# Kernel tuning notes

Hardware: AMD Instinct MI355X
Metric: run time of the kernel (lower is better)

Reference implementation:

```python
import jax, jax.numpy as jnp
import numpy as np

V, NB, NJ, NP, NK = 6890, 10, 24, 207, 19
PARENTS = np.array([-1, 0, 0, 0, 1, 2, 3, 4, 5, 6, 7, 8, 9, 9, 9, 12, 13, 14, 16, 17, 18, 19, 20, 21])


def setup_inputs():
    key = jax.random.key(0)
    ks = jax.random.split(key, 9)
    B = 1024
    beta = jax.random.normal(ks[0], (B, NB), jnp.float32)
    theta = jax.random.normal(ks[1], (B, NJ * 3), jnp.float32) * 0.3  # axis-angle per joint
    trans = jax.random.normal(ks[2], (B, 3), jnp.float32)
    v_template = jax.random.normal(ks[3], (V, 3), jnp.float32)
    shapedirs = jax.random.normal(ks[4], (NB, V * 3), jnp.float32) * 0.03
    Jr = jax.random.uniform(ks[5], (V, NJ), jnp.float32)
    J_regressor = Jr / jnp.sum(Jr, axis=0, keepdims=True)
    posedirs = jax.random.normal(ks[6], (NP, V * 3), jnp.float32) * 0.01
    jr = jax.random.uniform(ks[7], (V, NK), jnp.float32)
    joint_regressor = jr / jnp.sum(jr, axis=0, keepdims=True)
    w = jax.random.uniform(ks[8], (V, NJ), jnp.float32)
    weights = w / jnp.sum(w, axis=1, keepdims=True)  # LBS weights, rows sum to 1
    return dict(beta=beta, theta=theta, trans=trans, v_template=v_template,
                shapedirs=shapedirs, J_regressor=J_regressor, posedirs=posedirs,
                joint_regressor=joint_regressor, weights=weights)


def batch_rodrigues(theta):
    # theta: (N,3) axis-angle -> (N,3,3) rotation matrices via quaternions (HMR-style)
    angle = jnp.linalg.norm(theta + 1e-8, axis=1, keepdims=True)
    half = angle * 0.5
    v = (theta / angle) * jnp.sin(half)
    quat = jnp.concatenate([jnp.cos(half), v], axis=1)
    quat = quat / jnp.linalg.norm(quat, axis=1, keepdims=True)
    w, x, y, z = quat[:, 0], quat[:, 1], quat[:, 2], quat[:, 3]
    rot = jnp.stack([
        1 - 2 * (y * y + z * z), 2 * (x * y - w * z), 2 * (x * z + w * y),
        2 * (x * y + w * z), 1 - 2 * (x * x + z * z), 2 * (y * z - w * x),
        2 * (x * z - w * y), 2 * (y * z + w * x), 1 - 2 * (x * x + y * y)], axis=1)
    return rot.reshape(-1, 3, 3)


def batch_global_rigid_transformation(Rs, J):
    # Rs: (B,24,3,3), J: (B,24,3); rotate_base=True
    B = Rs.shape[0]
    rot_x = jnp.array([[1., 0., 0.], [0., -1., 0.], [0., 0., -1.]], jnp.float32)
    root_R = Rs[:, 0] @ rot_x

    def make_A(R, t):  # (B,3,3),(B,3) -> (B,4,4)
        top = jnp.concatenate([R, t[:, :, None]], axis=2)
        bot = jnp.broadcast_to(jnp.array([0., 0., 0., 1.], jnp.float32), (B, 1, 4))
        return jnp.concatenate([top, bot], axis=1)

    results = [make_A(root_R, J[:, 0])]
    for i in range(1, NJ):  # fixed 24-joint kinematic chain
        t = J[:, i] - J[:, PARENTS[i]]
        results.append(results[PARENTS[i]] @ make_A(Rs[:, i], t))
    res = jnp.stack(results, axis=1)  # (B,24,4,4)
    new_J = res[:, :, :3, 3]
    j_w0 = jnp.concatenate([J, jnp.zeros_like(J[:, :, :1])], axis=2)  # (B,24,4), homo w=0
    init_bone = jnp.einsum('bjrc,bjc->bjr', res, j_w0)
    A = res.at[:, :, :, 3].add(-init_bone)  # subtract only last column (matches F.pad trick)
    return new_J, A


def reference(beta, theta, trans, v_template, shapedirs, J_regressor, posedirs, joint_regressor, weights):
    B = beta.shape[0]
    v_shaped = (beta @ shapedirs).reshape(B, V, 3) + v_template
    J = jnp.einsum('bvc,vj->bjc', v_shaped, J_regressor)  # (B,24,3)
    Rs = batch_rodrigues(theta.reshape(-1, 3)).reshape(B, NJ, 3, 3)
    pose_feature = (Rs[:, 1:] - jnp.eye(3, dtype=Rs.dtype)).reshape(B, NP)
    v_posed = (pose_feature @ posedirs).reshape(B, V, 3) + v_shaped
    _, A = batch_global_rigid_transformation(Rs, J)
    T = jnp.einsum('vj,bjrc->bvrc', weights, A)  # (B,V,4,4) per-vertex skinning transforms
    homo = jnp.concatenate([v_posed, jnp.ones((B, V, 1), v_posed.dtype)], axis=2)
    verts = jnp.einsum('bvrc,bvc->bvr', T, homo)[:, :, :3] + trans[:, None, :]
    joints = jnp.einsum('bvc,vk->bkc', verts, joint_regressor)  # (B,19,3)
    return joints
```

## Files before the change

kernel.cpp:

```cpp
#include <hip/hip_runtime.h>
#include <hip/hip_bf16.h>

constexpr int Vn   = 6890;
constexpr int VC3  = 20670;
constexpr int KP   = 6912;
constexpr int NKB  = 216;
constexpr int QT   = 224;
constexpr int NMG  = 14;
constexpr int NCOL = 480;
constexpr int WR   = 1440;
constexpr int MC   = 1368;
constexpr int KSEG = 8;
constexpr int NG3  = 88;

using bf16x8  = __attribute__((ext_vector_type(8))) short;
using floatx4 = __attribute__((ext_vector_type(4))) float;

__device__ __forceinline__ unsigned short f2bf(float f) {
    unsigned int u = __float_as_uint(f);
    unsigned int r = (u + 0x7FFFu + ((u >> 16) & 1u)) >> 16;
    return (unsigned short)r;
}

__global__ __launch_bounds__(256) void k0_build(
    const float* __restrict__ vt, const float* __restrict__ sdirs,
    const float* __restrict__ pdirs, const float* __restrict__ Jreg,
    const float* __restrict__ jreg, const float* __restrict__ wts,
    unsigned short* __restrict__ Af, unsigned short* __restrict__ Bf)
{
    int bx = blockIdx.x, t = threadIdx.x;
    if (bx < QT * 27) {
        int q = bx / 27, v = (bx % 27) * 256 + t;
        float f[3] = {0.f, 0.f, 0.f};
        if (v < Vn) {
            if (q == 0) { f[0] = f[1] = f[2] = 1.f; }
            else {
                const float* src = nullptr;
                if (q == 1) src = vt;
                else if (q >= 2 && q < 12)   src = sdirs + (size_t)(q - 2) * VC3;
                else if (q >= 12 && q < 219) src = pdirs + (size_t)(q - 12) * VC3;
                if (src) { f[0] = src[3 * v]; f[1] = src[3 * v + 1]; f[2] = src[3 * v + 2]; }
            }
        }
        int mg = q >> 4, kb = v >> 5;
        size_t off = (size_t)((q & 15) + ((v >> 3) & 3) * 16) * 8 + (v & 7);
        #pragma unroll
        for (int c = 0; c < 3; ++c)
            Af[((size_t)(c * NMG + mg) * NKB + kb) * 512 + off] = f2bf(f[c]);
        return;
    }
    bx -= QT * 27;
    int v0 = bx * 64;
    __shared__ float js[64 * 19], wsh[64 * 24], Jsh[64 * 24];
    for (int i = t; i < 64 * 19; i += 256)
        js[i] = (v0 * 19 + i < Vn * 19) ? jreg[v0 * 19 + i] : 0.f;
    for (int i = t; i < 64 * 24; i += 256) {
        wsh[i] = (v0 * 24 + i < Vn * 24) ? wts[v0 * 24 + i] : 0.f;
        Jsh[i] = (v0 * 24 + i < Vn * 24) ? Jreg[v0 * 24 + i] : 0.f;
    }
    __syncthreads();
    for (int s = t; s < 4096; s += 256) {
        int col = s >> 3, vg = s & 7;
        int kb = (v0 >> 5) + (vg >> 2);
        bf16x8 o;
        #pragma unroll
        for (int j = 0; j < 8; ++j) {
            int vl = vg * 8 + j;
            float val = 0.f;
            if (col < 456)      val = js[vl * 19 + col / 24] * wsh[vl * 24 + col % 24];
            else if (col < 480) val = Jsh[vl * 24 + (col - 456)];
            o[j] = (short)f2bf(val);
        }
        *(bf16x8*)(Bf + ((size_t)(col >> 4) * NKB + kb) * 512
                      + (size_t)((col & 15) + (vg & 3) * 16) * 8) = o;
    }
}

__device__ __forceinline__ void k1_load(bf16x8 (&a)[2], bf16x8 (&b)[4],
    const unsigned short* __restrict__ ap, const unsigned short* __restrict__ bp, int i)
{
    a[0] = *(const bf16x8*)(ap + (size_t)(0 * NKB + i) * 512);
    a[1] = *(const bf16x8*)(ap + (size_t)(1 * NKB + i) * 512);
    b[0] = *(const bf16x8*)(bp + (size_t)(0 * NKB + i) * 512);
    b[1] = *(const bf16x8*)(bp + (size_t)(1 * NKB + i) * 512);
    b[2] = *(const bf16x8*)(bp + (size_t)(2 * NKB + i) * 512);
    b[3] = *(const bf16x8*)(bp + (size_t)(3 * NKB + i) * 512);
}

__global__ __launch_bounds__(64) void k1_mfma(
    const unsigned short* __restrict__ Af, const unsigned short* __restrict__ Bf,
    float* __restrict__ P)
{
    int l = threadIdx.x;
    int wid = blockIdx.x;
    int kseg = wid / 168; int r = wid % 168;
    int c = r / 56; r %= 56;
    int mt = r >> 3, nt = r & 7;
    int kb0 = kseg * 27;

    const unsigned short* ap = Af + ((size_t)(c * NMG + mt * 2) * NKB + kb0) * 512 + l * 8;
    const unsigned short* bp = Bf + ((size_t)(nt * 4) * NKB + kb0) * 512 + l * 8;

    floatx4 acc[2][4];
    #pragma unroll
    for (int mi = 0; mi < 2; ++mi)
        #pragma unroll
        for (int ni = 0; ni < 4; ++ni) acc[mi][ni] = floatx4{0.f, 0.f, 0.f, 0.f};

    bf16x8 a[4][2], b[4][4];
    k1_load(a[0], b[0], ap, bp, 0);
    k1_load(a[1], b[1], ap, bp, 1);
    k1_load(a[2], b[2], ap, bp, 2);
    #pragma unroll
    for (int i = 0; i < 27; ++i) {
        int pf = (i + 3 < 27) ? i + 3 : 26;
        k1_load(a[(i + 3) & 3], b[(i + 3) & 3], ap, bp, pf);
        bf16x8 (&ac)[2] = a[i & 3];
        bf16x8 (&bc)[4] = b[i & 3];
        #pragma unroll
        for (int mi = 0; mi < 2; ++mi)
            #pragma unroll
            for (int ni = 0; ni < 4; ++ni)
                acc[mi][ni] = __builtin_amdgcn_mfma_f32_16x16x32_bf16(ac[mi], bc[ni], acc[mi][ni], 0, 0, 0);
    }
    float* Ps = P + (size_t)kseg * WR * QT;
    int lr = l & 15, r0 = (l >> 4) * 4;
    #pragma unroll
    for (int mi = 0; mi < 2; ++mi)
        #pragma unroll
        for (int ni = 0; ni < 4; ++ni) {
            int col = nt * 64 + ni * 16 + lr;
            if (col < NCOL) {
                int q0 = mt * 32 + mi * 16 + r0;
                #pragma unroll
                for (int rr = 0; rr < 4; ++rr)
                    Ps[(size_t)(col * 3 + c) * QT + q0 + rr] = acc[mi][ni][rr];
            }
        }
}

constexpr int RB = 158;
__global__ __launch_bounds__(256) void k12_reduce_prep(
    const float* __restrict__ P,
    const float* __restrict__ beta, const float* __restrict__ theta,
    float* __restrict__ WtF, unsigned short* __restrict__ Wb3,
    unsigned short* __restrict__ xbf, float* __restrict__ RAg, float* __restrict__ tAg)
{
    int t = threadIdx.x;
    if (blockIdx.x < RB) {
        int g = blockIdx.x * 256 + t;
        if (g >= WR * 28) return;
        int colc = g / 28, qg = g % 28, q0 = qg * 8;
        float v[8] = {0, 0, 0, 0, 0, 0, 0, 0};
        #pragma unroll
        for (int s = 0; s < KSEG; ++s) {
            const float4* p = (const float4*)(P + ((size_t)s * WR + colc) * QT + q0);
            float4 x0 = p[0], x1 = p[1];
            v[0] += x0.x; v[1] += x0.y; v[2] += x0.z; v[3] += x0.w;
            v[4] += x1.x; v[5] += x1.y; v[6] += x1.z; v[7] += x1.w;
        }
        float4* wp = (float4*)(WtF + (size_t)colc * QT + q0);
        wp[0] = make_float4(v[0], v[1], v[2], v[3]);
        wp[1] = make_float4(v[4], v[5], v[6], v[7]);
        if (colc < NG3 * 16) {
            bf16x8 o;
            #pragma unroll
            for (int j = 0; j < 8; ++j)
                o[j] = (short)((colc < MC) ? f2bf(v[j]) : 0);
            int ng3 = colc >> 4, kb3 = q0 >> 5;
            *(bf16x8*)(Wb3 + ((size_t)ng3 * 7 + kb3) * 512
                           + (size_t)((colc & 15) + ((q0 >> 3) & 3) * 16) * 8) = o;
        }
        return;
    }
    int b = blockIdx.x - RB;
    __shared__ float Rs[24][9];
    __shared__ float Jl[24][3];
    __shared__ float resR[24][9];
    __shared__ float rest[24][3];
    __shared__ float bet[10];

    if (t < 10) bet[t] = beta[b * 10 + t];
    if (t < 24) {
        float t0 = theta[b * 72 + t * 3 + 0];
        float t1 = theta[b * 72 + t * 3 + 1];
        float t2 = theta[b * 72 + t * 3 + 2];
        float e0 = t0 + 1e-8f, e1 = t1 + 1e-8f, e2 = t2 + 1e-8f;
        float angle = sqrtf(e0 * e0 + e1 * e1 + e2 * e2);
        float half = 0.5f * angle;
        float sh = sinf(half), ch = cosf(half);
        float s = sh / angle;
        float qx = t0 * s, qy = t1 * s, qz = t2 * s;
        float qn = sqrtf(ch * ch + qx * qx + qy * qy + qz * qz);
        float w = ch / qn, x = qx / qn, y = qy / qn, z = qz / qn;
        Rs[t][0] = 1.f - 2.f * (y * y + z * z);
        Rs[t][1] = 2.f * (x * y - w * z);
        Rs[t][2] = 2.f * (x * z + w * y);
        Rs[t][3] = 2.f * (x * y + w * z);
        Rs[t][4] = 1.f - 2.f * (x * x + z * z);
        Rs[t][5] = 2.f * (y * z - w * x);
        Rs[t][6] = 2.f * (x * z + -w * y);
        Rs[t][7] = 2.f * (y * z + w * x);
        Rs[t][8] = 1.f - 2.f * (x * x + y * y);
    }
    __syncthreads();
    if (t < 72) {
        int colc = 1368 + t;
        float acc = 0.f;
        #pragma unroll
        for (int s = 0; s < KSEG; ++s)
            acc += P[((size_t)s * WR + colc) * QT + 1];
        #pragma unroll
        for (int n = 0; n < 10; ++n) {
            float cf = 0.f;
            #pragma unroll
            for (int s = 0; s < KSEG; ++s)
                cf += P[((size_t)s * WR + colc) * QT + 2 + n];
            acc += bet[n] * cf;
        }
        Jl[t / 3][t % 3] = acc;
    }
    if (t < QT) {
        int q = t;
        float xv = 0.f;
        if (q == 1) xv = 1.f;
        else if (q >= 2 && q < 12) xv = bet[q - 2];
        else if (q >= 12 && q < 219) {
            int p = q - 12;
            int jj = 1 + p / 9, e = p % 9;
            float rr = Rs[jj][e];
            if (e == 0 || e == 4 || e == 8) rr -= 1.f;
            xv = rr;
        }
        int bg = b >> 4, kb3 = q >> 5;
        xbf[((size_t)bg * 7 + kb3) * 512
            + (size_t)((b & 15) + ((q >> 3) & 3) * 16) * 8 + (q & 7)] = f2bf(xv);
    }
    __syncthreads();
    if (t == 0) {
        const int par[24] = {-1,0,0,0,1,2,3,4,5,6,7,8,9,9,9,12,13,14,16,17,18,19,20,21};
        #pragma unroll
        for (int rr = 0; rr < 3; ++rr) {
            resR[0][rr * 3 + 0] =  Rs[0][rr * 3 + 0];
            resR[0][rr * 3 + 1] = -Rs[0][rr * 3 + 1];
            resR[0][rr * 3 + 2] = -Rs[0][rr * 3 + 2];
            rest[0][rr] = Jl[0][rr];
        }
        for (int i = 1; i < 24; ++i) {
            int p = par[i];
            float t0 = Jl[i][0] - Jl[p][0];
            float t1 = Jl[i][1] - Jl[p][1];
            float t2 = Jl[i][2] - Jl[p][2];
            #pragma unroll
            for (int rr = 0; rr < 3; ++rr) {
                float a0 = resR[p][rr * 3 + 0], a1 = resR[p][rr * 3 + 1], a2 = resR[p][rr * 3 + 2];
                resR[i][rr * 3 + 0] = a0 * Rs[i][0] + a1 * Rs[i][3] + a2 * Rs[i][6];
                resR[i][rr * 3 + 1] = a0 * Rs[i][1] + a1 * Rs[i][4] + a2 * Rs[i][7];
                resR[i][rr * 3 + 2] = a0 * Rs[i][2] + a1 * Rs[i][5] + a2 * Rs[i][8];
                rest[i][rr] = a0 * t0 + a1 * t1 + a2 * t2 + rest[p][rr];
            }
        }
    }
    __syncthreads();
    if (t < 216) RAg[(size_t)b * 216 + t] = resR[t / 9][t % 9];
    if (t < 72) {
        int j = t / 3, c = t % 3;
        tAg[(size_t)b * 72 + t] = rest[j][c]
            - (resR[j][c * 3 + 0] * Jl[j][0] + resR[j][c * 3 + 1] * Jl[j][1]
             + resR[j][c * 3 + 2] * Jl[j][2]);
    }
}

__device__ __forceinline__ void k3_load(bf16x8 (&a)[2], bf16x8 (&b)[4],
    const unsigned short* __restrict__ ap, const unsigned short* __restrict__ bp, int i)
{
    a[0] = *(const bf16x8*)(ap + (size_t)(0 * 7 + i) * 512);
    a[1] = *(const bf16x8*)(ap + (size_t)(1 * 7 + i) * 512);
    b[0] = *(const bf16x8*)(bp + (size_t)(0 * 7 + i) * 512);
    b[1] = *(const bf16x8*)(bp + (size_t)(1 * 7 + i) * 512);
    b[2] = *(const bf16x8*)(bp + (size_t)(2 * 7 + i) * 512);
    b[3] = *(const bf16x8*)(bp + (size_t)(3 * 7 + i) * 512);
}

__global__ __launch_bounds__(256) void k3_mfma(
    const unsigned short* __restrict__ xbf, const unsigned short* __restrict__ Wb3,
    float* __restrict__ Mg)
{
    int w = threadIdx.x >> 6, l = threadIdx.x & 63;
    int wm = w & 1, wn = w >> 1;
    int bt = blockIdx.x / 11, ct = blockIdx.x % 11;
    int bg0 = bt * 4 + wm * 2;
    int ng0 = ct * 8 + wn * 4;

    const unsigned short* ap = xbf + (size_t)bg0 * 7 * 512 + l * 8;
    const unsigned short* bp = Wb3 + (size_t)ng0 * 7 * 512 + l * 8;

    floatx4 acc[2][4];
    #pragma unroll
    for (int mi = 0; mi < 2; ++mi)
        #pragma unroll
        for (int ni = 0; ni < 4; ++ni) acc[mi][ni] = floatx4{0.f, 0.f, 0.f, 0.f};

    bf16x8 a[3][2], b[3][4];
    k3_load(a[0], b[0], ap, bp, 0);
    k3_load(a[1], b[1], ap, bp, 1);
    #pragma unroll
    for (int i = 0; i < 7; ++i) {
        int pf = (i + 2 < 7) ? i + 2 : 6;
        k3_load(a[(i + 2) % 3], b[(i + 2) % 3], ap, bp, pf);
        bf16x8 (&ac)[2] = a[i % 3];
        bf16x8 (&bc)[4] = b[i % 3];
        #pragma unroll
        for (int mi = 0; mi < 2; ++mi)
            #pragma unroll
            for (int ni = 0; ni < 4; ++ni)
                acc[mi][ni] = __builtin_amdgcn_mfma_f32_16x16x32_bf16(ac[mi], bc[ni], acc[mi][ni], 0, 0, 0);
    }
    int lr = l & 15, r0 = (l >> 4) * 4;
    #pragma unroll
    for (int mi = 0; mi < 2; ++mi)
        #pragma unroll
        for (int ni = 0; ni < 4; ++ni) {
            int cc = ct * 128 + wn * 64 + ni * 16 + lr;
            if (cc < MC) {
                int brow = bt * 64 + wm * 32 + mi * 16 + r0;
                #pragma unroll
                for (int rr = 0; rr < 4; ++rr)
                    Mg[(size_t)(brow + rr) * MC + cc] = acc[mi][ni][rr];
            }
        }
}

__global__ __launch_bounds__(256) void k4_combine(
    const float* __restrict__ Mg, const float* __restrict__ RAg,
    const float* __restrict__ tAg, const float* __restrict__ WtF,
    const float* __restrict__ trans, float* __restrict__ out)
{
    __shared__ float w1s[456];
    __shared__ float Ms[4 * MC];
    __shared__ float RAs[4 * 216];
    __shared__ float tAs[4 * 72];
    int tid = threadIdx.x;
    int b0 = blockIdx.x * 4;
    for (int i = tid; i < 456; i += 256) w1s[i] = WtF[(size_t)i * 3 * QT];
    for (int i = tid; i < 4 * MC; i += 256) Ms[i] = Mg[(size_t)b0 * MC + i];
    for (int i = tid; i < 4 * 216; i += 256) RAs[i] = RAg[(size_t)b0 * 216 + i];
    for (int i = tid; i < 4 * 72; i += 256) tAs[i] = tAg[(size_t)b0 * 72 + i];
    __syncthreads();
    if (tid < 228) {
        int lb = tid / 57, kc = tid % 57;
        int k = kc / 3, c = kc % 3;
        int b = b0 + lb;
        float acc = trans[b * 3 + c];
        const float* Mrow = Ms + lb * MC;
        const float* RAr  = RAs + lb * 216;
        const float* tAr  = tAs + lb * 72;
        #pragma unroll
        for (int j = 0; j < 24; ++j) {
            int kj = k * 24 + j;
            float m0 = Mrow[kj * 3 + 0], m1 = Mrow[kj * 3 + 1], m2 = Mrow[kj * 3 + 2];
            acc += RAr[j * 9 + c * 3 + 0] * m0
                 + RAr[j * 9 + c * 3 + 1] * m1
                 + RAr[j * 9 + c * 3 + 2] * m2
                 + tAr[j * 3 + c] * w1s[kj];
        }
        out[b * 57 + kc] = acc;
    }
}

extern "C" void kernel_launch(void* const* d_in, const int* in_sizes, int n_in,
                              void* d_out, int out_size, void* d_ws, size_t ws_size,
                              hipStream_t stream)
{
    const float* beta  = (const float*)d_in[0];
    const float* theta = (const float*)d_in[1];
    const float* trans = (const float*)d_in[2];
    const float* vt    = (const float*)d_in[3];
    const float* sdirs = (const float*)d_in[4];
    const float* Jreg  = (const float*)d_in[5];
    const float* pdirs = (const float*)d_in[6];
    const float* jreg  = (const float*)d_in[7];
    const float* wts   = (const float*)d_in[8];
    float* out = (float*)d_out;
    int B = in_sizes[0] / 10;

    unsigned short* Af  = (unsigned short*)d_ws;
    unsigned short* Bf  = Af + (size_t)3 * NMG * NKB * 512;
    unsigned short* Wb3 = Bf + (size_t)32 * NKB * 512;
    unsigned short* xbf = Wb3 + (size_t)NG3 * 7 * 512;
    float* P   = (float*)(xbf + (size_t)64 * 7 * 512);
    float* WtF = P + (size_t)KSEG * WR * QT;
    float* RAg = WtF + (size_t)WR * QT;
    float* tAg = RAg + (size_t)B * 216;
    float* Mg  = tAg + (size_t)B * 72;

    k0_build<<<dim3(QT * 27 + 108), 256, 0, stream>>>(
        vt, sdirs, pdirs, Jreg, jreg, wts, Af, Bf);
    k1_mfma<<<dim3(168 * KSEG), 64, 0, stream>>>(Af, Bf, P);
    k12_reduce_prep<<<dim3(RB + B), 256, 0, stream>>>(
        P, beta, theta, WtF, Wb3, xbf, RAg, tAg);
    k3_mfma<<<dim3((B / 64) * 11), 256, 0, stream>>>(xbf, Wb3, Mg);
    k4_combine<<<dim3(B / 4), 256, 0, stream>>>(Mg, RAg, tAg, WtF, trans, out);
}
```

Before: 153.6 us.

## Vectorize weight packing, share B tiles across xyz, split reduce/prep, transpose k3

The packing kernel now has each thread load 8 vertices with float2 reads and write whole bf16x8 fragments, where before it issued scalar strided stores. k1 computes all three coordinate channels in one wave so each B fragment is reused three times, with 12 K segments and double buffering, and writes results as vector stores. The fused reduce/prep kernel is split into a reduce kernel and a 64-thread per-batch prep kernel that reads the already reduced WtF instead of summing partials. k3 swaps operand roles so its outputs can be stored as float4. This adds a kernel launch and more partial-sum traffic from the extra segments.

```diff
diff --git a/kernel.cpp b/kernel.cpp
--- a/kernel.cpp
+++ b/kernel.cpp
@@ -3,14 +3,14 @@
 
 constexpr int Vn   = 6890;
 constexpr int VC3  = 20670;
-constexpr int KP   = 6912;
 constexpr int NKB  = 216;
 constexpr int QT   = 224;
 constexpr int NMG  = 14;
 constexpr int NCOL = 480;
 constexpr int WR   = 1440;
 constexpr int MC   = 1368;
-constexpr int KSEG = 8;
+constexpr int KSEG = 12;
+constexpr int KCH  = 18;
 constexpr int NG3  = 88;
 
 using bf16x8  = __attribute__((ext_vector_type(8))) short;
@@ -29,27 +29,43 @@
     unsigned short* __restrict__ Af, unsigned short* __restrict__ Bf)
 {
     int bx = blockIdx.x, t = threadIdx.x;
-    if (bx < QT * 27) {
-        int q = bx / 27, v = (bx % 27) * 256 + t;
-        float f[3] = {0.f, 0.f, 0.f};
-        if (v < Vn) {
-            if (q == 0) { f[0] = f[1] = f[2] = 1.f; }
-            else {
-                const float* src = nullptr;
-                if (q == 1) src = vt;
-                else if (q >= 2 && q < 12)   src = sdirs + (size_t)(q - 2) * VC3;
-                else if (q >= 12 && q < 219) src = pdirs + (size_t)(q - 12) * VC3;
-                if (src) { f[0] = src[3 * v]; f[1] = src[3 * v + 1]; f[2] = src[3 * v + 2]; }
+    if (bx < 756) {
+        int g = bx * 256 + t;
+        int q = g / 864, u = g % 864;
+        int v0 = u * 8, base = 3 * v0;
+        float buf[24];
+        if (q == 0) {
+            #pragma unroll
+            for (int i = 0; i < 24; ++i) buf[i] = (v0 + i / 3 < Vn) ? 1.f : 0.f;
+        } else {
+            const float* src = nullptr;
+            if (q == 1) src = vt;
+            else if (q >= 2 && q < 12)   src = sdirs + (size_t)(q - 2) * VC3;
+            else if (q >= 12 && q < 219) src = pdirs + (size_t)(q - 12) * VC3;
+            if (src && base + 23 < VC3) {
+                #pragma unroll
+                for (int i = 0; i < 12; ++i) {
+                    float2 f = *(const float2*)(src + base + 2 * i);
+                    buf[2 * i] = f.x; buf[2 * i + 1] = f.y;
+                }
+            } else {
+                #pragma unroll
+                for (int i = 0; i < 24; ++i)
+                    buf[i] = (src && base + i < VC3) ? src[base + i] : 0.f;
             }
         }
-        int mg = q >> 4, kb = v >> 5;
-        size_t off = (size_t)((q & 15) + ((v >> 3) & 3) * 16) * 8 + (v & 7);
-        #pragma unroll
-        for (int c = 0; c < 3; ++c)
-            Af[((size_t)(c * NMG + mg) * NKB + kb) * 512 + off] = f2bf(f[c]);
+        int kb = u >> 2, quad = u & 3, mg = q >> 4;
+        size_t foff = (size_t)((q & 15) + quad * 16) * 8;
+        #pragma unroll
+        for (int c = 0; c < 3; ++c) {
+            bf16x8 o;
+            #pragma unroll
+            for (int j = 0; j < 8; ++j) o[j] = (short)f2bf(buf[3 * j + c]);
+            *(bf16x8*)(Af + ((size_t)(c * NMG + mg) * NKB + kb) * 512 + foff) = o;
+        }
         return;
     }
-    bx -= QT * 27;
+    bx -= 756;
     int v0 = bx * 64;
     __shared__ float js[64 * 19], wsh[64 * 24], Jsh[64 * 24];
     for (int i = t; i < 64 * 19; i += 256)
@@ -76,115 +92,117 @@
     }
 }
 
-__device__ __forceinline__ void k1_load(bf16x8 (&a)[2], bf16x8 (&b)[4],
-    const unsigned short* __restrict__ ap, const unsigned short* __restrict__ bp, int i)
-{
-    a[0] = *(const bf16x8*)(ap + (size_t)(0 * NKB + i) * 512);
-    a[1] = *(const bf16x8*)(ap + (size_t)(1 * NKB + i) * 512);
-    b[0] = *(const bf16x8*)(bp + (size_t)(0 * NKB + i) * 512);
-    b[1] = *(const bf16x8*)(bp + (size_t)(1 * NKB + i) * 512);
-    b[2] = *(const bf16x8*)(bp + (size_t)(2 * NKB + i) * 512);
-    b[3] = *(const bf16x8*)(bp + (size_t)(3 * NKB + i) * 512);
-}
-
 __global__ __launch_bounds__(64) void k1_mfma(
     const unsigned short* __restrict__ Af, const unsigned short* __restrict__ Bf,
     float* __restrict__ P)
 {
     int l = threadIdx.x;
     int wid = blockIdx.x;
-    int kseg = wid / 168; int r = wid % 168;
-    int c = r / 56; r %= 56;
+    int kseg = wid / 56, r = wid % 56;
     int mt = r >> 3, nt = r & 7;
-    int kb0 = kseg * 27;
-
-    const unsigned short* ap = Af + ((size_t)(c * NMG + mt * 2) * NKB + kb0) * 512 + l * 8;
+    int kb0 = kseg * KCH;
+
+    const unsigned short* ap = Af + ((size_t)(mt * 2) * NKB + kb0) * 512 + l * 8;
     const unsigned short* bp = Bf + ((size_t)(nt * 4) * NKB + kb0) * 512 + l * 8;
 
-    floatx4 acc[2][4];
-    #pragma unroll
-    for (int mi = 0; mi < 2; ++mi)
-        #pragma unroll
-        for (int ni = 0; ni < 4; ++ni) acc[mi][ni] = floatx4{0.f, 0.f, 0.f, 0.f};
-
-    bf16x8 a[4][2], b[4][4];
-    k1_load(a[0], b[0], ap, bp, 0);
-    k1_load(a[1], b[1], ap, bp, 1);
-    k1_load(a[2], b[2], ap, bp, 2);
-    #pragma unroll
-    for (int i = 0; i < 27; ++i) {
-        int pf = (i + 3 < 27) ? i + 3 : 26;
-        k1_load(a[(i + 3) & 3], b[(i + 3) & 3], ap, bp, pf);
-        bf16x8 (&ac)[2] = a[i & 3];
-        bf16x8 (&bc)[4] = b[i & 3];
+    floatx4 acc[3][2][4];
+    #pragma unroll
+    for (int c = 0; c < 3; ++c)
         #pragma unroll
         for (int mi = 0; mi < 2; ++mi)
             #pragma unroll
+            for (int ni = 0; ni < 4; ++ni) acc[c][mi][ni] = floatx4{0.f, 0.f, 0.f, 0.f};
+
+    bf16x8 a[2][3][2], b[2][4];
+    #pragma unroll
+    for (int c = 0; c < 3; ++c)
+        #pragma unroll
+        for (int mi = 0; mi < 2; ++mi)
+            a[0][c][mi] = *(const bf16x8*)(ap + ((size_t)(c * NMG + mi) * NKB) * 512);
+    #pragma unroll
+    for (int ni = 0; ni < 4; ++ni)
+        b[0][ni] = *(const bf16x8*)(bp + ((size_t)ni * NKB) * 512);
+
+    for (int i = 0; i < KCH; ++i) {
+        int s = i & 1;
+        if (i + 1 < KCH) {
+            #pragma unroll
+            for (int c = 0; c < 3; ++c)
+                #pragma unroll
+                for (int mi = 0; mi < 2; ++mi)
+                    a[s ^ 1][c][mi] = *(const bf16x8*)(ap + ((size_t)(c * NMG + mi) * NKB + i + 1) * 512);
+            #pragma unroll
             for (int ni = 0; ni < 4; ++ni)
-                acc[mi][ni] = __builtin_amdgcn_mfma_f32_16x16x32_bf16(ac[mi], bc[ni], acc[mi][ni], 0, 0, 0);
-    }
-    float* Ps = P + (size_t)kseg * WR * QT;
-    int lr = l & 15, r0 = (l >> 4) * 4;
-    #pragma unroll
-    for (int mi = 0; mi < 2; ++mi)
-        #pragma unroll
-        for (int ni = 0; ni < 4; ++ni) {
-            int col = nt * 64 + ni * 16 + lr;
-            if (col < NCOL) {
-                int q0 = mt * 32 + mi * 16 + r0;
+                b[s ^ 1][ni] = *(const bf16x8*)(bp + ((size_t)ni * NKB + i + 1) * 512);
+        }
+        #pragma unroll
+        for (int c = 0; c < 3; ++c)
+            #pragma unroll
+            for (int mi = 0; mi < 2; ++mi)
                 #pragma unroll
-                for (int rr = 0; rr < 4; ++rr)
-                    Ps[(size_t)(col * 3 + c) * QT + q0 + rr] = acc[mi][ni][rr];
+                for (int ni = 0; ni < 4; ++ni)
+                    acc[c][mi][ni] = __builtin_amdgcn_mfma_f32_16x16x32_bf16(
+                        a[s][c][mi], b[s][ni], acc[c][mi][ni], 0, 0, 0);
+    }
+    float* base = P + (size_t)kseg * WR * QT;
+    int lr = l & 15, rq = (l >> 4) * 4;
+    #pragma unroll
+    for (int c = 0; c < 3; ++c)
+        #pragma unroll
+        for (int mi = 0; mi < 2; ++mi)
+            #pragma unroll
+            for (int ni = 0; ni < 4; ++ni) {
+                int col = nt * 64 + ni * 16 + lr;
+                if (col < NCOL) {
+                    int q0 = mt * 32 + mi * 16 + rq;
+                    *(floatx4*)(base + (size_t)(col * 3 + c) * QT + q0) = acc[c][mi][ni];
+                }
             }
-        }
-}
-
-constexpr int RB = 158;
-__global__ __launch_bounds__(256) void k12_reduce_prep(
-    const float* __restrict__ P,
+}
+
+__global__ __launch_bounds__(256) void kr_reduce(
+    const float* __restrict__ P, float* __restrict__ WtF, unsigned short* __restrict__ Wb3)
+{
+    int g = blockIdx.x * 256 + threadIdx.x;
+    if (g >= WR * 28) return;
+    int colc = g / 28, q0 = (g % 28) * 8;
+    float v[8] = {0, 0, 0, 0, 0, 0, 0, 0};
+    for (int s = 0; s < KSEG; ++s) {
+        const float4* p = (const float4*)(P + ((size_t)s * WR + colc) * QT + q0);
+        float4 x0 = p[0], x1 = p[1];
+        v[0] += x0.x; v[1] += x0.y; v[2] += x0.z; v[3] += x0.w;
+        v[4] += x1.x; v[5] += x1.y; v[6] += x1.z; v[7] += x1.w;
+    }
+    float4* wp = (float4*)(WtF + (size_t)colc * QT + q0);
+    wp[0] = make_float4(v[0], v[1], v[2], v[3]);
+    wp[1] = make_float4(v[4], v[5], v[6], v[7]);
+    if (colc < NG3 * 16) {
+        bf16x8 o;
+        #pragma unroll
+        for (int j = 0; j < 8; ++j)
+            o[j] = (short)((colc < MC) ? f2bf(v[j]) : 0);
+        *(bf16x8*)(Wb3 + ((size_t)(colc >> 4) * 7 + (q0 >> 5)) * 512
+                       + (size_t)((colc & 15) + ((q0 >> 3) & 3) * 16) * 8) = o;
+    }
+}
+
+__global__ __launch_bounds__(64) void kp_prep(
     const float* __restrict__ beta, const float* __restrict__ theta,
-    float* __restrict__ WtF, unsigned short* __restrict__ Wb3,
+    const float* __restrict__ WtF,
     unsigned short* __restrict__ xbf, float* __restrict__ RAg, float* __restrict__ tAg)
 {
-    int t = threadIdx.x;
-    if (blockIdx.x < RB) {
-        int g = blockIdx.x * 256 + t;
-        if (g >= WR * 28) return;
-        int colc = g / 28, qg = g % 28, q0 = qg * 8;
-        float v[8] = {0, 0, 0, 0, 0, 0, 0, 0};
-        #pragma unroll
-        for (int s = 0; s < KSEG; ++s) {
-            const float4* p = (const float4*)(P + ((size_t)s * WR + colc) * QT + q0);
-            float4 x0 = p[0], x1 = p[1];
-            v[0] += x0.x; v[1] += x0.y; v[2] += x0.z; v[3] += x0.w;
-            v[4] += x1.x; v[5] += x1.y; v[6] += x1.z; v[7] += x1.w;
-        }
-        float4* wp = (float4*)(WtF + (size_t)colc * QT + q0);
-        wp[0] = make_float4(v[0], v[1], v[2], v[3]);
-        wp[1] = make_float4(v[4], v[5], v[6], v[7]);
-        if (colc < NG3 * 16) {
-            bf16x8 o;
-            #pragma unroll
-            for (int j = 0; j < 8; ++j)
-                o[j] = (short)((colc < MC) ? f2bf(v[j]) : 0);
-            int ng3 = colc >> 4, kb3 = q0 >> 5;
-            *(bf16x8*)(Wb3 + ((size_t)ng3 * 7 + kb3) * 512
-                           + (size_t)((colc & 15) + ((q0 >> 3) & 3) * 16) * 8) = o;
-        }
-        return;
-    }
-    int b = blockIdx.x - RB;
+    int b = blockIdx.x, lane = threadIdx.x;
     __shared__ float Rs[24][9];
     __shared__ float Jl[24][3];
     __shared__ float resR[24][9];
     __shared__ float rest[24][3];
     __shared__ float bet[10];
 
-    if (t < 10) bet[t] = beta[b * 10 + t];
-    if (t < 24) {
-        float t0 = theta[b * 72 + t * 3 + 0];
-        float t1 = theta[b * 72 + t * 3 + 1];
-        float t2 = theta[b * 72 + t * 3 + 2];
+    if (lane < 10) bet[lane] = beta[b * 10 + lane];
+    if (lane < 24) {
+        float t0 = theta[b * 72 + lane * 3 + 0];
+        float t1 = theta[b * 72 + lane * 3 + 1];
+        float t2 = theta[b * 72 + lane * 3 + 2];
         float e0 = t0 + 1e-8f, e1 = t1 + 1e-8f, e2 = t2 + 1e-8f;
         float angle = sqrtf(e0 * e0 + e1 * e1 + e2 * e2);
         float half = 0.5f * angle;
@@ -193,35 +211,25 @@
         float qx = t0 * s, qy = t1 * s, qz = t2 * s;
         float qn = sqrtf(ch * ch + qx * qx + qy * qy + qz * qz);
         float w = ch / qn, x = qx / qn, y = qy / qn, z = qz / qn;
-        Rs[t][0] = 1.f - 2.f * (y * y + z * z);
-        Rs[t][1] = 2.f * (x * y - w * z);
-        Rs[t][2] = 2.f * (x * z + w * y);
-        Rs[t][3] = 2.f * (x * y + w * z);
-        Rs[t][4] = 1.f - 2.f * (x * x + z * z);
-        Rs[t][5] = 2.f * (y * z - w * x);
-        Rs[t][6] = 2.f * (x * z + -w * y);
-        Rs[t][7] = 2.f * (y * z + w * x);
-        Rs[t][8] = 1.f - 2.f * (x * x + y * y);
-    }
-    __syncthreads();
-    if (t < 72) {
-        int colc = 1368 + t;
-        float acc = 0.f;
-        #pragma unroll
-        for (int s = 0; s < KSEG; ++s)
-            acc += P[((size_t)s * WR + colc) * QT + 1];
-        #pragma unroll
-        for (int n = 0; n < 10; ++n) {
-            float cf = 0.f;
-            #pragma unroll
-            for (int s = 0; s < KSEG; ++s)
-                cf += P[((size_t)s * WR + colc) * QT + 2 + n];
-            acc += bet[n] * cf;
-        }
-        Jl[t / 3][t % 3] = acc;
-    }
-    if (t < QT) {
-        int q = t;
+        Rs[lane][0] = 1.f - 2.f * (y * y + z * z);
+        Rs[lane][1] = 2.f * (x * y - w * z);
+        Rs[lane][2] = 2.f * (x * z + w * y);
+        Rs[lane][3] = 2.f * (x * y + w * z);
+        Rs[lane][4] = 1.f - 2.f * (x * x + z * z);
+        Rs[lane][5] = 2.f * (y * z - w * x);
+        Rs[lane][6] = 2.f * (x * z - w * y);
+        Rs[lane][7] = 2.f * (y * z + w * x);
+        Rs[lane][8] = 1.f - 2.f * (x * x + y * y);
+    }
+    __syncthreads();
+    for (int idx = lane; idx < 72; idx += 64) {
+        const float* colp = WtF + (size_t)(1368 + idx) * QT;
+        float acc = colp[1];
+        #pragma unroll
+        for (int n = 0; n < 10; ++n) acc += bet[n] * colp[2 + n];
+        Jl[idx / 3][idx % 3] = acc;
+    }
+    for (int q = lane; q < QT; q += 64) {
         float xv = 0.f;
         if (q == 1) xv = 1.f;
         else if (q >= 2 && q < 12) xv = bet[q - 2];
@@ -232,12 +240,11 @@
             if (e == 0 || e == 4 || e == 8) rr -= 1.f;
             xv = rr;
         }
-        int bg = b >> 4, kb3 = q >> 5;
-        xbf[((size_t)bg * 7 + kb3) * 512
+        xbf[((size_t)(b >> 4) * 7 + (q >> 5)) * 512
             + (size_t)((b & 15) + ((q >> 3) & 3) * 16) * 8 + (q & 7)] = f2bf(xv);
     }
     __syncthreads();
-    if (t == 0) {
+    if (lane == 0) {
         const int par[24] = {-1,0,0,0,1,2,3,4,5,6,7,8,9,9,9,12,13,14,16,17,18,19,20,21};
         #pragma unroll
         for (int rr = 0; rr < 3; ++rr) {
@@ -262,38 +269,27 @@
         }
     }
     __syncthreads();
-    if (t < 216) RAg[(size_t)b * 216 + t] = resR[t / 9][t % 9];
-    if (t < 72) {
-        int j = t / 3, c = t % 3;
-        tAg[(size_t)b * 72 + t] = rest[j][c]
+    for (int idx = lane; idx < 216; idx += 64)
+        RAg[(size_t)b * 216 + idx] = resR[idx / 9][idx % 9];
+    for (int idx = lane; idx < 72; idx += 64) {
+        int j = idx / 3, c = idx % 3;
+        tAg[(size_t)b * 72 + idx] = rest[j][c]
             - (resR[j][c * 3 + 0] * Jl[j][0] + resR[j][c * 3 + 1] * Jl[j][1]
              + resR[j][c * 3 + 2] * Jl[j][2]);
     }
 }
 
-__device__ __forceinline__ void k3_load(bf16x8 (&a)[2], bf16x8 (&b)[4],
-    const unsigned short* __restrict__ ap, const unsigned short* __restrict__ bp, int i)
-{
-    a[0] = *(const bf16x8*)(ap + (size_t)(0 * 7 + i) * 512);
-    a[1] = *(const bf16x8*)(ap + (size_t)(1 * 7 + i) * 512);
-    b[0] = *(const bf16x8*)(bp + (size_t)(0 * 7 + i) * 512);
-    b[1] = *(const bf16x8*)(bp + (size_t)(1 * 7 + i) * 512);
-    b[2] = *(const bf16x8*)(bp + (size_t)(2 * 7 + i) * 512);
-    b[3] = *(const bf16x8*)(bp + (size_t)(3 * 7 + i) * 512);
-}
-
 __global__ __launch_bounds__(256) void k3_mfma(
-    const unsigned short* __restrict__ xbf, const unsigned short* __restrict__ Wb3,
+    const unsigned short* __restrict__ Wb3, const unsigned short* __restrict__ xbf,
     float* __restrict__ Mg)
 {
     int w = threadIdx.x >> 6, l = threadIdx.x & 63;
     int wm = w & 1, wn = w >> 1;
-    int bt = blockIdx.x / 11, ct = blockIdx.x % 11;
-    int bg0 = bt * 4 + wm * 2;
-    int ng0 = ct * 8 + wn * 4;
-
-    const unsigned short* ap = xbf + (size_t)bg0 * 7 * 512 + l * 8;
-    const unsigned short* bp = Wb3 + (size_t)ng0 * 7 * 512 + l * 8;
+    int ct = blockIdx.x % 22, bt = blockIdx.x / 22;
+    int mg0 = ct * 4 + wm * 2;
+    int bg0 = bt * 8 + wn * 4;
+    const unsigned short* ap = Wb3 + (size_t)mg0 * 7 * 512 + l * 8;
+    const unsigned short* bp = xbf + (size_t)bg0 * 7 * 512 + l * 8;
 
     floatx4 acc[2][4];
     #pragma unroll
@@ -301,33 +297,32 @@
         #pragma unroll
         for (int ni = 0; ni < 4; ++ni) acc[mi][ni] = floatx4{0.f, 0.f, 0.f, 0.f};
 
-    bf16x8 a[3][2], b[3][4];
-    k3_load(a[0], b[0], ap, bp, 0);
-    k3_load(a[1], b[1], ap, bp, 1);
-    #pragma unroll
-    for (int i = 0; i < 7; ++i) {
-        int pf = (i + 2 < 7) ? i + 2 : 6;
-        k3_load(a[(i + 2) % 3], b[(i + 2) % 3], ap, bp, pf);
-        bf16x8 (&ac)[2] = a[i % 3];
-        bf16x8 (&bc)[4] = b[i % 3];
-        #pragma unroll
-        for (int mi = 0; mi < 2; ++mi)
-            #pragma unroll
-            for (int ni = 0; ni < 4; ++ni)
-                acc[mi][ni] = __builtin_amdgcn_mfma_f32_16x16x32_bf16(ac[mi], bc[ni], acc[mi][ni], 0, 0, 0);
-    }
-    int lr = l & 15, r0 = (l >> 4) * 4;
+    #pragma unroll
+    for (int kk = 0; kk < 7; ++kk) {
+        bf16x8 a0 = *(const bf16x8*)(ap + (size_t)(0 * 7 + kk) * 512);
+        bf16x8 a1 = *(const bf16x8*)(ap + (size_t)(1 * 7 + kk) * 512);
+        bf16x8 b0 = *(const bf16x8*)(bp + (size_t)(0 * 7 + kk) * 512);
+        bf16x8 b1 = *(const bf16x8*)(bp + (size_t)(1 * 7 + kk) * 512);
+        bf16x8 b2 = *(const bf16x8*)(bp + (size_t)(2 * 7 + kk) * 512);
+        bf16x8 b3 = *(const bf16x8*)(bp + (size_t)(3 * 7 + kk) * 512);
+        acc[0][0] = __builtin_amdgcn_mfma_f32_16x16x32_bf16(a0, b0, acc[0][0], 0, 0, 0);
+        acc[0][1] = __builtin_amdgcn_mfma_f32_16x16x32_bf16(a0, b1, acc[0][1], 0, 0, 0);
+        acc[0][2] = __builtin_amdgcn_mfma_f32_16x16x32_bf16(a0, b2, acc[0][2], 0, 0, 0);
+        acc[0][3] = __builtin_amdgcn_mfma_f32_16x16x32_bf16(a0, b3, acc[0][3], 0, 0, 0);
+        acc[1][0] = __builtin_amdgcn_mfma_f32_16x16x32_bf16(a1, b0, acc[1][0], 0, 0, 0);
+        acc[1][1] = __builtin_amdgcn_mfma_f32_16x16x32_bf16(a1, b1, acc[1][1], 0, 0, 0);
+        acc[1][2] = __builtin_amdgcn_mfma_f32_16x16x32_bf16(a1, b2, acc[1][2], 0, 0, 0);
+        acc[1][3] = __builtin_amdgcn_mfma_f32_16x16x32_bf16(a1, b3, acc[1][3], 0, 0, 0);
+    }
+    int lr = l & 15, rq = (l >> 4) * 4;
     #pragma unroll
     for (int mi = 0; mi < 2; ++mi)
         #pragma unroll
         for (int ni = 0; ni < 4; ++ni) {
-            int cc = ct * 128 + wn * 64 + ni * 16 + lr;
-            if (cc < MC) {
-                int brow = bt * 64 + wm * 32 + mi * 16 + r0;
-                #pragma unroll
-                for (int rr = 0; rr < 4; ++rr)
-                    Mg[(size_t)(brow + rr) * MC + cc] = acc[mi][ni][rr];
-            }
+            int b  = bt * 128 + wn * 64 + ni * 16 + lr;
+            int cc = (mg0 + mi) * 16 + rq;
+            if (cc < MC)
+                *(floatx4*)(Mg + (size_t)b * MC + cc) = acc[mi][ni];
         }
 }
 
@@ -394,11 +389,11 @@
     float* tAg = RAg + (size_t)B * 216;
     float* Mg  = tAg + (size_t)B * 72;
 
-    k0_build<<<dim3(QT * 27 + 108), 256, 0, stream>>>(
+    k0_build<<<dim3(756 + 108), 256, 0, stream>>>(
         vt, sdirs, pdirs, Jreg, jreg, wts, Af, Bf);
-    k1_mfma<<<dim3(168 * KSEG), 64, 0, stream>>>(Af, Bf, P);
-    k12_reduce_prep<<<dim3(RB + B), 256, 0, stream>>>(
-        P, beta, theta, WtF, Wb3, xbf, RAg, tAg);
-    k3_mfma<<<dim3((B / 64) * 11), 256, 0, stream>>>(xbf, Wb3, Mg);
+    k1_mfma<<<dim3(56 * KSEG), 64, 0, stream>>>(Af, Bf, P);
+    kr_reduce<<<dim3(158), 256, 0, stream>>>(P, WtF, Wb3);
+    kp_prep<<<dim3(B), 64, 0, stream>>>(beta, theta, WtF, xbf, RAg, tAg);
+    k3_mfma<<<dim3((B / 128) * 22), 256, 0, stream>>>(Wb3, xbf, Mg);
     k4_combine<<<dim3(B / 4), 256, 0, stream>>>(Mg, RAg, tAg, WtF, trans, out);
 }
```

After: 166.8 us. 8.6% more time.
